# Kernel optimization log

Measured on AMD Instinct MI355X. Metric: run time of the kernel, lower is better.

The kernel has to match this reference:

```python
import jax, jax.numpy as jnp
import numpy as np

B, L, D = 2, 2048, 2048
NH, NKV = 16, 8
HD = D // NH            # 128
GQ = NH // NKV          # queries per kv head
THETA = 10000.0
SCALE = HD ** -0.5


def rope_tables(seq_len, dim, theta):
    inv_freq = 1.0 / theta ** (jnp.arange(0, dim, 2, dtype=jnp.float32) / dim)
    t = jnp.arange(seq_len, dtype=jnp.float32)
    freqs = jnp.outer(t, inv_freq)              # [L, dim/2]
    emb = jnp.concatenate([freqs, freqs], -1)   # [L, dim]
    return jnp.cos(emb), jnp.sin(emb)


def rotate_half(x):
    x1, x2 = jnp.split(x, 2, axis=-1)
    return jnp.concatenate([-x2, x1], -1)


def setup_inputs() -> dict:
    key = jax.random.key(0)
    ks = jax.random.split(key, 5)
    s = 0.02
    return {
        "x": jax.random.normal(ks[0], (B, L, D), jnp.float32),
        "Wq": jax.random.normal(ks[1], (NH * HD, D), jnp.float32) * s,
        "Wk": jax.random.normal(ks[2], (NKV * HD, D), jnp.float32) * s,
        "Wv": jax.random.normal(ks[3], (NKV * HD, D), jnp.float32) * s,
        "Wo": jax.random.normal(ks[4], (D, D), jnp.float32) * s,
    }


def reference(x, Wq, Wk, Wv, Wo):
    b, l, d = x.shape
    q = (x @ Wq.T).reshape(b, l, NH, HD).transpose(0, 2, 1, 3)    # [B,NH,L,HD]
    k = (x @ Wk.T).reshape(b, l, NKV, HD).transpose(0, 2, 1, 3)   # [B,NKV,L,HD]
    v = (x @ Wv.T).reshape(b, l, NKV, HD).transpose(0, 2, 1, 3)

    cos, sin = rope_tables(l, HD, THETA)                           # [L,HD]
    q = q * cos + rotate_half(q) * sin
    k = k * cos + rotate_half(k) * sin

    # GQA without materializing expanded K/V: group queries per kv head
    qg = q.reshape(b, NKV, GQ, l, HD)
    scores = jnp.einsum('bgrld,bgmd->bgrlm', qg, k) * SCALE        # [B,NKV,GQ,L,L]
    causal = jnp.triu(jnp.ones((l, l), bool), k=1)
    scores = jnp.where(causal, -jnp.inf, scores)
    attn = jax.nn.softmax(scores.astype(jnp.float32), axis=-1).astype(q.dtype)
    out = jnp.einsum('bgrlm,bgmd->bgrld', attn, v)                 # [B,NKV,GQ,L,HD]
    out = out.reshape(b, NH, l, HD).transpose(0, 2, 1, 3).reshape(b, l, d)
    return out @ Wo.T
```

## Files before the change

kernel.cpp:

```cpp
#include <hip/hip_runtime.h>
#include <cmath>

using u16 = unsigned short;
typedef u16    u16x4  __attribute__((ext_vector_type(4)));
typedef u16    u16x8  __attribute__((ext_vector_type(8)));
typedef __bf16 bf16x8 __attribute__((ext_vector_type(8)));
typedef float  f32x4  __attribute__((ext_vector_type(4)));

constexpr int Bc  = 2;
constexpr int Lc  = 2048;
constexpr int Dc  = 2048;
constexpr int NHc = 16;
constexpr int NKVc= 8;
constexpr int HDc = 128;

__device__ __forceinline__ u16 f2b(float f) {
  union { float f; unsigned u; } v; v.f = f;
  unsigned r = v.u + 0x7FFFu + ((v.u >> 16) & 1u);
  return (u16)(r >> 16);
}
__device__ __forceinline__ u16 f2b_fast(float f) {
  union { float f; unsigned u; } v; v.f = f;
  return (u16)((v.u + 0x8000u) >> 16);
}
__device__ __forceinline__ float b2f(u16 s) {
  union { unsigned u; float f; } v; v.u = ((unsigned)s) << 16;
  return v.f;
}
__device__ __forceinline__ bf16x8 ld_frag(const u16* p) {
  u16x8 u = *(const u16x8*)p;
  return __builtin_bit_cast(bf16x8, u);
}
__device__ __forceinline__ void gld_lds16(u16* ldst, const u16* gsrc) {
  __builtin_amdgcn_global_load_lds(
      (const __attribute__((address_space(1))) void*)gsrc,
      (__attribute__((address_space(3))) void*)ldst, 16, 0, 0);
}

__global__ void cvt_f32_bf16(const float* __restrict__ src, u16* __restrict__ dst, int n) {
  int i = (blockIdx.x * blockDim.x + threadIdx.x) * 4;
  if (i >= n) return;
  float4 v = *(const float4*)&src[i];
  u16x4 o = { f2b(v.x), f2b(v.y), f2b(v.z), f2b(v.w) };
  *(u16x4*)&dst[i] = o;
}

__global__ void cvt_w3(const float* __restrict__ Wq, const float* __restrict__ Wk,
                       const float* __restrict__ Wv, u16* __restrict__ dst) {
  const int n1 = Dc * Dc;
  const int n2 = n1 + (NKVc*HDc) * Dc;
  const int n3 = n2 + (NKVc*HDc) * Dc;
  int i = (blockIdx.x * blockDim.x + threadIdx.x) * 4;
  if (i >= n3) return;
  const float* src; int off;
  if (i < n1)      { src = Wq; off = i; }
  else if (i < n2) { src = Wk; off = i - n1; }
  else             { src = Wv; off = i - n2; }
  float4 v = *(const float4*)&src[off];
  u16x4 o = { f2b(v.x), f2b(v.y), f2b(v.z), f2b(v.w) };
  *(u16x4*)&dst[i] = o;
}

#define MFMA_(a, b, c) __builtin_amdgcn_mfma_f32_16x16x32_bf16(a, b, c, 0, 0, 0)
#define BAR()   __builtin_amdgcn_s_barrier()
#define LGKM0() { __asm__ volatile("s_waitcnt lgkmcnt(0)" ::: "memory"); \
                  __builtin_amdgcn_sched_barrier(0); }
#define VMC4()  __asm__ volatile("s_waitcnt vmcnt(4)" ::: "memory")
#define VMC0()  __asm__ volatile("s_waitcnt vmcnt(0)" ::: "memory")
#define PRIO1() __builtin_amdgcn_s_setprio(1)
#define PRIO0() __builtin_amdgcn_s_setprio(0)

#define STG(lb, gp, goff, h, kc)                                          \
  { _Pragma("unroll")                                                     \
    for (int i_ = 0; i_ < 2; ++i_) {                                      \
      int c_ = wave + (i_ << 3);                                          \
      gld_lds16((lb) + (h) * 8192 + c_ * 512,                             \
                (gp) + (goff) + (size_t)(h) * 262144 + (size_t)c_ * 16384 + (kc)); } }

#define RD_ALO(rp) { _Pragma("unroll") for (int mi_ = 0; mi_ < 4; ++mi_) { \
    aLo[mi_][0] = ld_frag((rp) + mi_*1024 + cg0);                          \
    aLo[mi_][1] = ld_frag((rp) + mi_*1024 + cg1); } }
#define RD_AHI(rp) { _Pragma("unroll") for (int mi_ = 0; mi_ < 4; ++mi_) { \
    aHi[mi_][0] = ld_frag((rp) + (4+mi_)*1024 + cg0);                      \
    aHi[mi_][1] = ld_frag((rp) + (4+mi_)*1024 + cg1); } }
#define RD_BLO(rp) { _Pragma("unroll") for (int ni_ = 0; ni_ < 2; ++ni_) { \
    bLo[ni_][0] = ld_frag((rp) + ni_*1024 + cg0);                          \
    bLo[ni_][1] = ld_frag((rp) + ni_*1024 + cg1); } }
#define RD_BHI(rp) { _Pragma("unroll") for (int ni_ = 0; ni_ < 2; ++ni_) { \
    bHi[ni_][0] = ld_frag((rp) + (2+ni_)*1024 + cg0);                      \
    bHi[ni_][1] = ld_frag((rp) + (2+ni_)*1024 + cg1); } }

#define QMFMA(MI0, NI0, AX, BX)                                                \
  { _Pragma("unroll")                                                          \
    for (int mi_ = 0; mi_ < 4; ++mi_) {                                        \
      _Pragma("unroll")                                                        \
      for (int ni_ = 0; ni_ < 2; ++ni_) {                                      \
        acc[(MI0)+mi_][(NI0)+ni_] =                                            \
            MFMA_(AX[mi_][0], BX[ni_][0], acc[(MI0)+mi_][(NI0)+ni_]);          \
        acc[(MI0)+mi_][(NI0)+ni_] =                                            \
            MFMA_(AX[mi_][1], BX[ni_][1], acc[(MI0)+mi_][(NI0)+ni_]); } } }

__global__ __launch_bounds__(512, 2) void gemm256_qkv(
    const u16* __restrict__ A, const u16* __restrict__ W,
    u16* __restrict__ Qp, u16* __restrict__ Kp, u16* __restrict__ Vtp, float qs)
{
  __shared__ u16 lds[65536];
  const int tid  = threadIdx.x;
  const int wave = tid >> 6, lane = tid & 63;
  const int quad = lane >> 4, l16 = lane & 15, t7 = l16 & 7;
  const int bid = blockIdx.x;
  const int swz = (bid & 7) * 32 + (bid >> 3);
  const int tx = swz & 15, ty = swz >> 4;
  const int m0 = ty * 256, n0 = tx * 256;
  const int wm = wave >> 2, wn = wave & 3;
  const int srow = lane >> 3;
  const int sx8  = ((lane & 7) ^ srow) << 3;

  u16* const A0L = lds;
  u16* const B0L = lds + 16384;
  u16* const A1L = lds + 32768;
  u16* const B1L = lds + 49152;

  const size_t aOff = (size_t)(m0 + srow) * 2048 + sx8;
  const size_t bOff = (size_t)(n0 + srow) * 2048 + sx8;

  const int cg0 = ((quad ^ t7) << 3);
  const int cg1 = (((quad ^ t7) ^ 4) << 3);
  const u16* const rA0 = A0L + wm * 8192 + l16 * 64;
  const u16* const rA1 = A1L + wm * 8192 + l16 * 64;
  const u16* const rB0 = B0L + wn * 4096 + l16 * 64;
  const u16* const rB1 = B1L + wn * 4096 + l16 * 64;

  f32x4 acc[8][4];
#pragma unroll
  for (int i = 0; i < 8; ++i)
#pragma unroll
    for (int j = 0; j < 4; ++j) acc[i][j] = {0.f, 0.f, 0.f, 0.f};
  bf16x8 aLo[4][2], aHi[4][2], bLo[2][2], bHi[2][2];

  STG(B0L, W, bOff, 0, 0);  STG(B0L, W, bOff, 1, 0);
  STG(A0L, A, aOff, 0, 0);  STG(A0L, A, aOff, 1, 0);
  STG(B1L, W, bOff, 0, 64); STG(B1L, W, bOff, 1, 64);
  VMC4();
  BAR();

  for (int it = 0; it < 16; ++it) {
    const int kc = it * 128;
    const bool g = (it < 15);
    RD_ALO(rA0); RD_BLO(rB0);
    STG(A1L, A, aOff, 0, kc + 64);
    LGKM0(); BAR();
    PRIO1(); QMFMA(0, 0, aLo, bLo); PRIO0();
    RD_BHI(rB0);
    STG(A1L, A, aOff, 1, kc + 64);
    LGKM0(); BAR();
    PRIO1(); QMFMA(0, 2, aLo, bHi); PRIO0();
    RD_AHI(rA0);
    if (g) STG(B0L, W, bOff, 0, kc + 128);
    LGKM0(); BAR();
    PRIO1(); QMFMA(4, 0, aHi, bLo); PRIO0();
    if (g) { STG(B0L, W, bOff, 1, kc + 128); VMC4(); }
    else   { VMC0(); }
    LGKM0(); BAR();
    PRIO1(); QMFMA(4, 2, aHi, bHi); PRIO0();
    RD_ALO(rA1); RD_BLO(rB1);
    if (g) STG(A0L, A, aOff, 0, kc + 128);
    LGKM0(); BAR();
    PRIO1(); QMFMA(0, 0, aLo, bLo); PRIO0();
    RD_BHI(rB1);
    if (g) STG(A0L, A, aOff, 1, kc + 128);
    LGKM0(); BAR();
    PRIO1(); QMFMA(0, 2, aLo, bHi); PRIO0();
    RD_AHI(rA1);
    if (g) STG(B1L, W, bOff, 0, kc + 192);
    LGKM0(); BAR();
    PRIO1(); QMFMA(4, 0, aHi, bLo); PRIO0();
    if (g) { STG(B1L, W, bOff, 1, kc + 192); VMC4(); }
    LGKM0(); BAR();
    PRIO1(); QMFMA(4, 2, aHi, bHi); PRIO0();
  }

  if (n0 < 3072) {
    u16* Cb; int ldc, nc0; float osc;
    if (n0 < 2048) { Cb = Qp; ldc = 2048; nc0 = n0; osc = qs; }
    else           { Cb = Kp; ldc = 1024; nc0 = n0 - 2048; osc = 1.f; }
    __syncthreads();
#pragma unroll
    for (int mi = 0; mi < 8; ++mi)
#pragma unroll
      for (int ni = 0; ni < 4; ++ni)
#pragma unroll
        for (int r = 0; r < 4; ++r) {
          int l = wm * 128 + mi * 16 + quad * 4 + r;
          int d = wn * 64 + ni * 16 + l16;
          int cgp = ((d >> 3) ^ (l & 31) ^ (l >> 5)) & 31;
          lds[l * 256 + (cgp << 3) + (d & 7)] = f2b(acc[mi][ni][r]);
        }
    __syncthreads();
    const int pg   = tid & 15;
    const int head = pg >> 3, cgl2 = pg & 7;
    const int cgL  = head * 16 + cgl2;
    const int cgH  = cgL + 8;
    float fr[8];
#pragma unroll
    for (int e = 0; e < 8; ++e)
      fr[e] = exp2f((float)(cgl2 * 8 + e) * (-13.287712379549449f / 64.f));
#pragma unroll
    for (int it2 = 0; it2 < 8; ++it2) {
      int row = (tid >> 4) + it2 * 32;
      int sx = (row & 31) ^ (row >> 5);
      u16x8 vlo = *(const u16x8*)&lds[row * 256 + (((cgL ^ sx) & 31) << 3)];
      u16x8 vhi = *(const u16x8*)&lds[row * 256 + (((cgH ^ sx) & 31) << 3)];
      float lseq = (float)((m0 + row) & (Lc - 1));
      u16x8 olo, ohi;
#pragma unroll
      for (int e = 0; e < 8; ++e) {
        float s, c;
        sincosf(lseq * fr[e], &s, &c);
        float x1 = b2f(vlo[e]), x2 = b2f(vhi[e]);
        olo[e] = f2b((x1 * c - x2 * s) * osc);
        ohi[e] = f2b((x2 * c + x1 * s) * osc);
      }
      size_t base = (size_t)(m0 + row) * ldc + nc0 + head * 128 + cgl2 * 8;
      *(u16x8*)&Cb[base]      = olo;
      *(u16x8*)&Cb[base + 64] = ohi;
    }
  } else {
    __syncthreads();
#pragma unroll
    for (int mi = 0; mi < 8; ++mi)
#pragma unroll
      for (int ni = 0; ni < 4; ++ni)
#pragma unroll
        for (int r = 0; r < 4; ++r) {
          int l = wm * 128 + mi * 16 + quad * 4 + r;
          int d = wn * 64 + ni * 16 + l16;
          int cgp = ((d >> 3) ^ (l & 31) ^ (l >> 5)) & 31;
          lds[l * 256 + (cgp << 3) + (d & 7)] = f2b(acc[mi][ni][r]);
        }
    __syncthreads();
    const int b    = m0 >> 11;
    const int hkv0 = (n0 - 3072) >> 7;
#pragma unroll
    for (int it2 = 0; it2 < 16; ++it2) {
      int sl = tid + it2 * 512;
      int dl = sl >> 5;
      int lc = (sl & 31) * 8;
      u16x8 v;
#pragma unroll
      for (int e = 0; e < 8; ++e) {
        int l = lc + e;
        int cgp = ((dl >> 3) ^ (l & 31) ^ (l >> 5)) & 31;
        v[e] = lds[l * 256 + (cgp << 3) + (dl & 7)];
      }
      const int hkv = hkv0 + (dl >> 7);
      const int d   = dl & 127;
      *(u16x8*)&Vtp[(((size_t)b * NKVc + hkv) * HDc + d) * (size_t)Lc + (m0 & (Lc - 1)) + lc] = v;
    }
  }
}
#undef STG
#undef RD_ALO
#undef RD_AHI
#undef RD_BLO
#undef RD_BHI
#undef QMFMA

__global__ __launch_bounds__(256) void gemm_out(
    const u16* __restrict__ A, const u16* __restrict__ W,
    float* __restrict__ Cf, int M, int N, int K)
{
  __shared__ u16 lds[16384];
  u16* lA = lds;
  u16* lB = lds + 8192;
  const int tid  = threadIdx.x;
  const int wave = tid >> 6, lane = tid & 63;
  const int quad = lane >> 4, l16 = lane & 15;
  const int t7   = l16 & 7;
  const int m0 = blockIdx.y * 128, n0 = blockIdx.x * 128;
  const int mw = (wave >> 1) * 64, nw = (wave & 1) * 64;
  const int r8 = lane >> 3;
  const int cgl = (lane & 7) ^ r8;

  f32x4 acc[4][4];
#pragma unroll
  for (int i = 0; i < 4; ++i)
#pragma unroll
    for (int j = 0; j < 4; ++j) acc[i][j] = {0.f, 0.f, 0.f, 0.f};

  for (int kt = 0; kt < K; kt += 64) {
#pragma unroll
    for (int cc = 0; cc < 4; ++cc) {
      int c = wave + cc * 4;
      gld_lds16(&lA[c * 512], &A[(size_t)(m0 + 8 * c + r8) * K + kt + cgl * 8]);
      gld_lds16(&lB[c * 512], &W[(size_t)(n0 + 8 * c + r8) * K + kt + cgl * 8]);
    }
    __syncthreads();
#pragma unroll
    for (int s = 0; s < 2; ++s) {
      bf16x8 af[4], bf[4];
#pragma unroll
      for (int i = 0; i < 4; ++i)
        af[i] = ld_frag(&lA[(mw + i*16 + l16) * 64 + ((quad + 4*s) ^ t7) * 8]);
#pragma unroll
      for (int j = 0; j < 4; ++j)
        bf[j] = ld_frag(&lB[(nw + j*16 + l16) * 64 + ((quad + 4*s) ^ t7) * 8]);
#pragma unroll
      for (int i = 0; i < 4; ++i)
#pragma unroll
        for (int j = 0; j < 4; ++j)
          acc[i][j] = __builtin_amdgcn_mfma_f32_16x16x32_bf16(af[i], bf[j], acc[i][j], 0, 0, 0);
    }
    __syncthreads();
  }

#pragma unroll
  for (int i = 0; i < 4; ++i)
#pragma unroll
    for (int j = 0; j < 4; ++j)
#pragma unroll
      for (int r = 0; r < 4; ++r) {
        int m = m0 + mw + i*16 + quad*4 + r;
        int n = n0 + nw + j*16 + l16;
        Cf[(size_t)m * N + n] = acc[i][j][r];
      }
}

__global__ __launch_bounds__(512) void flash_kernel(
    const u16* __restrict__ Q, const u16* __restrict__ K, const u16* __restrict__ Vt,
    u16* __restrict__ O)
{
  __shared__ u16 smem[41984];
  const int tid  = threadIdx.x;
  const int wave = tid >> 6, lane = tid & 63;
  const int quad = lane >> 4, l16 = lane & 15;
  const int hw = wave >> 2, wr = wave & 3;
  const int bhkv = blockIdx.x;
  const int b = bhkv >> 3, hkv = bhkv & 7;
  const int h = hkv * 2 + hw;

  const size_t kbase = ((size_t)b * Lc) * (NKVc * HDc) + (size_t)hkv * HDc;
  const size_t vbase = (((size_t)b * NKVc + hkv) * HDc) * (size_t)Lc;

  const int kr8 = lane >> 4;
  const int kcl = lane & 15;
  const int vr16 = lane >> 3;
  const int vkl  = lane & 7;

  u16* sP_w = smem + 32768 + wave * 1152;

  for (int pass = 0; pass < 2; ++pass) {
    const int qt = (pass == 0) ? (31 - (int)blockIdx.y) : (int)blockIdx.y;
    const int q0 = qt * 64;

    __syncthreads();
#pragma unroll
    for (int i = 0; i < 4; ++i) {
      int g = tid + i * 512;
      int row = g >> 4, cg = g & 15;
      int qh = hkv * 2 + (row >> 6);
      int rr = row & 63;
      *(u16x8*)&smem[row * 128 + (cg ^ (row & 15)) * 8] =
          *(const u16x8*)&Q[((size_t)(b * Lc + q0 + rr)) * Dc + (size_t)qh * HDc + cg * 8];
    }
    __syncthreads();
    bf16x8 qf[4];
#pragma unroll
    for (int ks = 0; ks < 4; ++ks)
      qf[ks] = ld_frag(&smem[(hw*64 + wr*16 + l16) * 128 + ((ks*4 + quad) ^ l16) * 8]);
    __syncthreads();

#pragma unroll
    for (int i = 0; i < 2; ++i) {
      int c = wave + i * 8;
      int row = c * 4 + kr8;
      gld_lds16(smem + c * 512,
                &K[kbase + (size_t)row * (NKVc*HDc) + (size_t)(kcl ^ (row & 15)) * 8]);
    }
#pragma unroll
    for (int i = 0; i < 2; ++i) {
      int c = wave + i * 8;
      int d = c * 8 + vr16;
      gld_lds16(smem + 16384 + c * 512,
                &Vt[vbase + (size_t)d * Lc + (size_t)(vkl ^ (d & 7)) * 8]);
    }

    f32x4 acc_o[8];
#pragma unroll
    for (int i = 0; i < 8; ++i) acc_o[i] = {0.f, 0.f, 0.f, 0.f};
    float ps[4] = {0.f, 0.f, 0.f, 0.f};

    for (int kt = 0; kt <= qt; ++kt) {
      const int kOff  = (kt & 1) ? 8192 : 0;
      const int kOffN = (kt & 1) ? 0 : 8192;
      const int vOff  = (kt & 1) ? 24576 : 16384;
      const int vOffN = (kt & 1) ? 16384 : 24576;

      __asm__ volatile("s_waitcnt vmcnt(2)\n\ts_barrier" ::: "memory");

      if (kt < qt) {
#pragma unroll
        for (int i = 0; i < 2; ++i) {
          int c = wave + i * 8;
          int row = (kt + 1) * 64 + c * 4 + kr8;
          gld_lds16(smem + kOffN + c * 512,
                    &K[kbase + (size_t)row * (NKVc*HDc) + (size_t)(kcl ^ (row & 15)) * 8]);
        }
      }

      const u16* sKc = smem + kOff;
      f32x4 accs[4];
#pragma unroll
      for (int n = 0; n < 4; ++n) accs[n] = {0.f, 0.f, 0.f, 0.f};
#pragma unroll
      for (int ks = 0; ks < 4; ++ks)
#pragma unroll
        for (int n = 0; n < 4; ++n) {
          bf16x8 kf = ld_frag(&sKc[(n*16 + l16) * 128 + ((ks*4 + quad) ^ l16) * 8]);
          accs[n] = __builtin_amdgcn_mfma_f32_16x16x32_bf16(qf[ks], kf, accs[n], 0, 0, 0);
        }

      const int qrow = q0 + wr*16 + quad*4;
      if (kt == qt) {
#pragma unroll
        for (int n = 0; n < 4; ++n) {
          int kg = kt*64 + n*16 + l16;
#pragma unroll
          for (int r = 0; r < 4; ++r)
            if (kg > qrow + r) accs[n][r] = -INFINITY;
        }
      }
#pragma unroll
      for (int n = 0; n < 4; ++n)
#pragma unroll
        for (int r = 0; r < 4; ++r) {
          float p = exp2f(accs[n][r]);
          accs[n][r] = p;
          ps[r] += p;
        }

#pragma unroll
      for (int n = 0; n < 4; ++n)
#pragma unroll
        for (int r = 0; r < 4; ++r)
          sP_w[(quad*4 + r) * 72 + n*16 + l16] = f2b_fast(accs[n][r]);

      if (kt < qt)
        __asm__ volatile("s_waitcnt vmcnt(2) lgkmcnt(0)\n\ts_barrier" ::: "memory");
      else
        __asm__ volatile("s_waitcnt vmcnt(0) lgkmcnt(0)\n\ts_barrier" ::: "memory");

      if (kt < qt) {
#pragma unroll
        for (int i = 0; i < 2; ++i) {
          int c = wave + i * 8;
          int d = c * 8 + vr16;
          gld_lds16(smem + vOffN + c * 512,
                    &Vt[vbase + (size_t)d * Lc + (kt+1)*64 + (size_t)(vkl ^ (d & 7)) * 8]);
        }
      }

      const u16* sVc = smem + vOff;
#pragma unroll
      for (int s2 = 0; s2 < 2; ++s2) {
        bf16x8 pf = ld_frag(&sP_w[l16 * 72 + s2*32 + quad*8]);
#pragma unroll
        for (int di = 0; di < 8; ++di) {
          bf16x8 vf = ld_frag(&sVc[(di*16 + l16) * 64 + ((s2*4 + quad) ^ (l16 & 7)) * 8]);
          acc_o[di] = __builtin_amdgcn_mfma_f32_16x16x32_bf16(pf, vf, acc_o[di], 0, 0, 0);
        }
      }
    }

#pragma unroll
    for (int off = 1; off < 16; off <<= 1)
#pragma unroll
      for (int r = 0; r < 4; ++r) ps[r] += __shfl_xor(ps[r], off);
    float inv[4];
#pragma unroll
    for (int r = 0; r < 4; ++r) inv[r] = 1.0f / ps[r];

#pragma unroll
    for (int di = 0; di < 8; ++di)
#pragma unroll
      for (int r = 0; r < 4; ++r) {
        int qrow = q0 + wr*16 + quad*4 + r;
        int d = di*16 + l16;
        float v = acc_o[di][r] * inv[r];
        O[((size_t)(b * Lc + qrow)) * Dc + (size_t)h * HDc + d] = f2b(v);
      }
  }
}

extern "C" void kernel_launch(void* const* d_in, const int* in_sizes, int n_in,
                              void* d_out, int out_size, void* d_ws, size_t ws_size,
                              hipStream_t stream)
{
  const float* x  = (const float*)d_in[0];
  const float* Wq = (const float*)d_in[1];
  const float* Wk = (const float*)d_in[2];
  const float* Wv = (const float*)d_in[3];
  const float* Wo = (const float*)d_in[4];
  float* out = (float*)d_out;

  const int M = Bc * Lc;
  u16* ws = (u16*)d_ws;
  u16* xb   = ws;
  u16* Ow   = xb;
  u16* Wcat = ws + (size_t)8 * 1024 * 1024;
  u16* Wob  = Wcat;
  u16* Qw   = Wcat + (size_t)8 * 1024 * 1024;
  u16* Kw   = Qw   + (size_t)8 * 1024 * 1024;
  u16* Vt   = Kw   + (size_t)4 * 1024 * 1024;

  const int nx = M * Dc;
  const int nq = Dc * Dc;
  const int nw3 = nq + 2 * (NKVc*HDc) * Dc;
  cvt_f32_bf16<<<nx/1024, 256, 0, stream>>>(x, xb, nx);
  cvt_w3<<<nw3/1024, 256, 0, stream>>>(Wq, Wk, Wv, Wcat);

  const float qs = 0.08838834764831845f * 1.4426950408889634f;
  gemm256_qkv<<<256, 512, 0, stream>>>(xb, Wcat, Qw, Kw, Vt, qs);

  flash_kernel<<<dim3(Bc*NKVc, 16), 512, 0, stream>>>(Qw, Kw, Vt, Ow);

  cvt_f32_bf16<<<nq/1024, 256, 0, stream>>>(Wo, Wob, nq);
  gemm_out<<<dim3(16, 32), 256, 0, stream>>>(Ow, Wob, out, M, Dc, Dc);
}
```

Before: 291.1 us.

## Widen flash attention key tile to 128 and merge input conversion kernels

The flash attention kernel now walks keys in 128-wide tiles instead of 64. That halves the loop trips, barriers and load-issue points per query tile, at the cost of roughly double the shared memory per block, a swizzled layout for the P buffer, and more masked wasted work on the diagonal tile. The separate x and QKV weight bf16 conversion kernels are merged into one launch to save a kernel launch. The larger LDS footprint may lower occupancy.

Result: slower. 297.6 us (+2.2%).

```diff
diff --git a/kernel.cpp b/kernel.cpp
--- a/kernel.cpp
+++ b/kernel.cpp
@@ -37,26 +37,32 @@
       (__attribute__((address_space(3))) void*)ldst, 16, 0, 0);
 }
 
+__global__ void cvt_xw3(const float* __restrict__ x,
+                        const float* __restrict__ Wq, const float* __restrict__ Wk,
+                        const float* __restrict__ Wv,
+                        u16* __restrict__ xb, u16* __restrict__ wcat) {
+  const int nx = Bc * Lc * Dc;
+  const int n1 = Dc * Dc;
+  const int n2 = n1 + (NKVc*HDc) * Dc;
+  int i = (blockIdx.x * blockDim.x + threadIdx.x) * 4;
+  const float* src; u16* dst; int off, dof;
+  if (i < nx) { src = x; dst = xb; off = i; dof = i; }
+  else {
+    int j = i - nx;
+    dst = wcat; dof = j;
+    if (j < n1)      { src = Wq; off = j; }
+    else if (j < n2) { src = Wk; off = j - n1; }
+    else             { src = Wv; off = j - n2; }
+  }
+  float4 v = *(const float4*)&src[off];
+  u16x4 o = { f2b(v.x), f2b(v.y), f2b(v.z), f2b(v.w) };
+  *(u16x4*)&dst[dof] = o;
+}
+
 __global__ void cvt_f32_bf16(const float* __restrict__ src, u16* __restrict__ dst, int n) {
   int i = (blockIdx.x * blockDim.x + threadIdx.x) * 4;
   if (i >= n) return;
   float4 v = *(const float4*)&src[i];
-  u16x4 o = { f2b(v.x), f2b(v.y), f2b(v.z), f2b(v.w) };
-  *(u16x4*)&dst[i] = o;
-}
-
-__global__ void cvt_w3(const float* __restrict__ Wq, const float* __restrict__ Wk,
-                       const float* __restrict__ Wv, u16* __restrict__ dst) {
-  const int n1 = Dc * Dc;
-  const int n2 = n1 + (NKVc*HDc) * Dc;
-  const int n3 = n2 + (NKVc*HDc) * Dc;
-  int i = (blockIdx.x * blockDim.x + threadIdx.x) * 4;
-  if (i >= n3) return;
-  const float* src; int off;
-  if (i < n1)      { src = Wq; off = i; }
-  else if (i < n2) { src = Wk; off = i - n1; }
-  else             { src = Wv; off = i - n2; }
-  float4 v = *(const float4*)&src[off];
   u16x4 o = { f2b(v.x), f2b(v.y), f2b(v.z), f2b(v.w) };
   *(u16x4*)&dst[i] = o;
 }
@@ -330,7 +336,7 @@
     const u16* __restrict__ Q, const u16* __restrict__ K, const u16* __restrict__ Vt,
     u16* __restrict__ O)
 {
-  __shared__ u16 smem[41984];
+  __shared__ u16 smem[81920];
   const int tid  = threadIdx.x;
   const int wave = tid >> 6, lane = tid & 63;
   const int quad = lane >> 4, l16 = lane & 15;
@@ -342,16 +348,17 @@
   const size_t kbase = ((size_t)b * Lc) * (NKVc * HDc) + (size_t)hkv * HDc;
   const size_t vbase = (((size_t)b * NKVc + hkv) * HDc) * (size_t)Lc;
 
-  const int kr8 = lane >> 4;
+  const int kr4 = lane >> 4;
   const int kcl = lane & 15;
-  const int vr16 = lane >> 3;
-  const int vkl  = lane & 7;
-
-  u16* sP_w = smem + 32768 + wave * 1152;
+  const int vr4 = lane >> 4;
+  const int vkl = lane & 15;
+
+  u16* sP_w = smem + 65536 + wave * 2048;
 
   for (int pass = 0; pass < 2; ++pass) {
     const int qt = (pass == 0) ? (31 - (int)blockIdx.y) : (int)blockIdx.y;
     const int q0 = qt * 64;
+    const int nkt = (qt >> 1) + 1;
 
     __syncthreads();
 #pragma unroll
@@ -360,28 +367,28 @@
       int row = g >> 4, cg = g & 15;
       int qh = hkv * 2 + (row >> 6);
       int rr = row & 63;
-      *(u16x8*)&smem[row * 128 + (cg ^ (row & 15)) * 8] =
+      *(u16x8*)&smem[row * 128 + ((cg ^ (row & 15)) << 3)] =
           *(const u16x8*)&Q[((size_t)(b * Lc + q0 + rr)) * Dc + (size_t)qh * HDc + cg * 8];
     }
     __syncthreads();
     bf16x8 qf[4];
 #pragma unroll
     for (int ks = 0; ks < 4; ++ks)
-      qf[ks] = ld_frag(&smem[(hw*64 + wr*16 + l16) * 128 + ((ks*4 + quad) ^ l16) * 8]);
-    __syncthreads();
-
-#pragma unroll
-    for (int i = 0; i < 2; ++i) {
+      qf[ks] = ld_frag(&smem[(hw*64 + wr*16 + l16) * 128 + (((ks*4 + quad) ^ l16) << 3)]);
+    __syncthreads();
+
+#pragma unroll
+    for (int i = 0; i < 4; ++i) {
       int c = wave + i * 8;
-      int row = c * 4 + kr8;
+      int row = c * 4 + kr4;
       gld_lds16(smem + c * 512,
                 &K[kbase + (size_t)row * (NKVc*HDc) + (size_t)(kcl ^ (row & 15)) * 8]);
     }
 #pragma unroll
-    for (int i = 0; i < 2; ++i) {
+    for (int i = 0; i < 4; ++i) {
       int c = wave + i * 8;
-      int d = c * 8 + vr16;
-      gld_lds16(smem + 16384 + c * 512,
+      int d = c * 4 + vr4;
+      gld_lds16(smem + 32768 + c * 512,
                 &Vt[vbase + (size_t)d * Lc + (size_t)(vkl ^ (d & 7)) * 8]);
     }
 
@@ -390,83 +397,81 @@
     for (int i = 0; i < 8; ++i) acc_o[i] = {0.f, 0.f, 0.f, 0.f};
     float ps[4] = {0.f, 0.f, 0.f, 0.f};
 
-    for (int kt = 0; kt <= qt; ++kt) {
-      const int kOff  = (kt & 1) ? 8192 : 0;
-      const int kOffN = (kt & 1) ? 0 : 8192;
-      const int vOff  = (kt & 1) ? 24576 : 16384;
-      const int vOffN = (kt & 1) ? 16384 : 24576;
-
-      __asm__ volatile("s_waitcnt vmcnt(2)\n\ts_barrier" ::: "memory");
-
-      if (kt < qt) {
-#pragma unroll
-        for (int i = 0; i < 2; ++i) {
+    for (int kt = 0; kt < nkt; ++kt) {
+      const bool more = (kt + 1 < nkt);
+      const int kOff  = (kt & 1) ? 16384 : 0;
+      const int kOffN = (kt & 1) ? 0 : 16384;
+      const int vOff  = 32768 + ((kt & 1) ? 16384 : 0);
+      const int vOffN = 32768 + ((kt & 1) ? 0 : 16384);
+
+      __asm__ volatile("s_waitcnt vmcnt(4)\n\ts_barrier" ::: "memory");
+
+      if (more) {
+#pragma unroll
+        for (int i = 0; i < 4; ++i) {
           int c = wave + i * 8;
-          int row = (kt + 1) * 64 + c * 4 + kr8;
+          int row = (kt + 1) * 128 + c * 4 + kr4;
           gld_lds16(smem + kOffN + c * 512,
                     &K[kbase + (size_t)row * (NKVc*HDc) + (size_t)(kcl ^ (row & 15)) * 8]);
         }
       }
 
       const u16* sKc = smem + kOff;
-      f32x4 accs[4];
-#pragma unroll
-      for (int n = 0; n < 4; ++n) accs[n] = {0.f, 0.f, 0.f, 0.f};
+      f32x4 accs[8];
+#pragma unroll
+      for (int n = 0; n < 8; ++n) accs[n] = {0.f, 0.f, 0.f, 0.f};
 #pragma unroll
       for (int ks = 0; ks < 4; ++ks)
 #pragma unroll
-        for (int n = 0; n < 4; ++n) {
-          bf16x8 kf = ld_frag(&sKc[(n*16 + l16) * 128 + ((ks*4 + quad) ^ l16) * 8]);
+        for (int n = 0; n < 8; ++n) {
+          bf16x8 kf = ld_frag(&sKc[(n*16 + l16) * 128 + (((ks*4 + quad) ^ l16) << 3)]);
           accs[n] = __builtin_amdgcn_mfma_f32_16x16x32_bf16(qf[ks], kf, accs[n], 0, 0, 0);
         }
 
       const int qrow = q0 + wr*16 + quad*4;
-      if (kt == qt) {
-#pragma unroll
-        for (int n = 0; n < 4; ++n) {
-          int kg = kt*64 + n*16 + l16;
+      if (kt == nkt - 1) {
+#pragma unroll
+        for (int n = 0; n < 8; ++n) {
+          int kg = kt*128 + n*16 + l16;
 #pragma unroll
           for (int r = 0; r < 4; ++r)
             if (kg > qrow + r) accs[n][r] = -INFINITY;
         }
       }
 #pragma unroll
-      for (int n = 0; n < 4; ++n)
+      for (int n = 0; n < 8; ++n) {
+        const int cgl = n*2 + (l16 >> 3);
 #pragma unroll
         for (int r = 0; r < 4; ++r) {
           float p = exp2f(accs[n][r]);
-          accs[n][r] = p;
           ps[r] += p;
-        }
-
-#pragma unroll
-      for (int n = 0; n < 4; ++n)
-#pragma unroll
-        for (int r = 0; r < 4; ++r)
-          sP_w[(quad*4 + r) * 72 + n*16 + l16] = f2b_fast(accs[n][r]);
-
-      if (kt < qt)
-        __asm__ volatile("s_waitcnt vmcnt(2) lgkmcnt(0)\n\ts_barrier" ::: "memory");
+          int prow = quad*4 + r;
+          sP_w[prow * 128 + (((cgl ^ (prow & 7)) << 3) + (l16 & 7))] = f2b_fast(p);
+        }
+      }
+
+      if (more)
+        __asm__ volatile("s_waitcnt vmcnt(4) lgkmcnt(0)\n\ts_barrier" ::: "memory");
       else
         __asm__ volatile("s_waitcnt vmcnt(0) lgkmcnt(0)\n\ts_barrier" ::: "memory");
 
-      if (kt < qt) {
-#pragma unroll
-        for (int i = 0; i < 2; ++i) {
+      if (more) {
+#pragma unroll
+        for (int i = 0; i < 4; ++i) {
           int c = wave + i * 8;
-          int d = c * 8 + vr16;
+          int d = c * 4 + vr4;
           gld_lds16(smem + vOffN + c * 512,
-                    &Vt[vbase + (size_t)d * Lc + (kt+1)*64 + (size_t)(vkl ^ (d & 7)) * 8]);
+                    &Vt[vbase + (size_t)d * Lc + (kt+1)*128 + (size_t)(vkl ^ (d & 7)) * 8]);
         }
       }
 
       const u16* sVc = smem + vOff;
 #pragma unroll
-      for (int s2 = 0; s2 < 2; ++s2) {
-        bf16x8 pf = ld_frag(&sP_w[l16 * 72 + s2*32 + quad*8]);
+      for (int s2 = 0; s2 < 4; ++s2) {
+        bf16x8 pf = ld_frag(&sP_w[l16 * 128 + (((s2*4 + quad) ^ (l16 & 7)) << 3)]);
 #pragma unroll
         for (int di = 0; di < 8; ++di) {
-          bf16x8 vf = ld_frag(&sVc[(di*16 + l16) * 64 + ((s2*4 + quad) ^ (l16 & 7)) * 8]);
+          bf16x8 vf = ld_frag(&sVc[(di*16 + l16) * 128 + (((s2*4 + quad) ^ (l16 & 7)) << 3)]);
           acc_o[di] = __builtin_amdgcn_mfma_f32_16x16x32_bf16(pf, vf, acc_o[di], 0, 0, 0);
         }
       }
@@ -489,6 +494,7 @@
         float v = acc_o[di][r] * inv[r];
         O[((size_t)(b * Lc + qrow)) * Dc + (size_t)h * HDc + d] = f2b(v);
       }
+    ps[0] = ps[1] = ps[2] = ps[3] = 0.f;
   }
 }
 
@@ -516,8 +522,7 @@
   const int nx = M * Dc;
   const int nq = Dc * Dc;
   const int nw3 = nq + 2 * (NKVc*HDc) * Dc;
-  cvt_f32_bf16<<<nx/1024, 256, 0, stream>>>(x, xb, nx);
-  cvt_w3<<<nw3/1024, 256, 0, stream>>>(Wq, Wk, Wv, Wcat);
+  cvt_xw3<<<(nx + nw3) / 1024, 256, 0, stream>>>(x, Wq, Wk, Wv, xb, Wcat);
 
   const float qs = 0.08838834764831845f * 1.4426950408889634f;
   gemm256_qkv<<<256, 512, 0, stream>>>(xb, Wcat, Qw, Kw, Vt, qs);
```
